# Performance work log

Hardware: AMD Instinct MI355X
Metric: run time of the kernel (lower is better)

## Reference

```python
import jax, jax.numpy as jnp
import numpy as np

B_SZ, SEQ, D_IN = 8, 4096, 1024
STATE, HEADS = 1024, 16
HEAD_DIM = STATE // HEADS
LN_EPS = 1e-5


def setup_inputs() -> dict:
    key = jax.random.key(0)
    ks = jax.random.split(key, 10)
    inp = {
        "x": jax.random.normal(ks[0], (B_SZ, SEQ, D_IN), dtype=jnp.float32),
        "W_in": jax.random.normal(ks[1], (STATE, D_IN), dtype=jnp.float32) * (1.0 / np.sqrt(D_IN)),
        "b_in": jnp.zeros((STATE,), dtype=jnp.float32),
        "log_A": jax.random.normal(ks[2], (HEADS, HEAD_DIM), dtype=jnp.float32) * 0.1 + 0.1,
        "B_p": jax.random.normal(ks[3], (HEADS, HEAD_DIM), dtype=jnp.float32) * 0.1 + 0.1,
        "C_p": jax.random.normal(ks[4], (HEADS, HEAD_DIM), dtype=jnp.float32) * 0.1 + 0.1,
        "W_out": jax.random.normal(ks[5], (STATE, STATE), dtype=jnp.float32) * (1.0 / np.sqrt(STATE)),
        "b_out": jnp.zeros((STATE,), dtype=jnp.float32),
        "gamma": jnp.ones((STATE,), dtype=jnp.float32),
        "beta": jnp.zeros((STATE,), dtype=jnp.float32),
    }
    return inp


def reference(x, W_in, b_in, log_A, B_p, C_p, W_out, b_out, gamma, beta):
    Bsz, S, _ = x.shape
    H, Dh = log_A.shape
    # input projection: (B,S,state)
    h = jnp.einsum("bsd,ed->bse", x, W_in) + b_in
    h = h.reshape(Bsz, S, H, Dh)
    decay = jnp.exp(-jax.nn.softplus(log_A))  # (H,Dh), time-invariant

    def step(s, xt):  # s,xt: (B,H,Dh)
        s = s * decay + B_p * xt
        return s, C_p * s

    s0 = jnp.zeros((Bsz, H, Dh), dtype=h.dtype)
    _, ys = jax.lax.scan(step, s0, jnp.swapaxes(h, 0, 1))  # ys: (S,B,H,Dh)
    y = jnp.swapaxes(ys, 0, 1).reshape(Bsz, S, H * Dh)
    out = jnp.einsum("bse,fe->bsf", y, W_out) + b_out
    # dropout in eval mode = identity; layer norm over last dim
    mu = out.mean(-1, keepdims=True)
    var = out.var(-1, keepdims=True)
    return (out - mu) * jax.lax.rsqrt(var + LN_EPS) * gamma + beta
```

## Files before the change

### kernel.cpp

```cpp
#include <hip/hip_runtime.h>

#define B_SZ  8
#define SEQ   4096
#define D_IN  1024
#define STATE 1024
#define M_TOT (B_SZ * SEQ)
#define LN_EPS 1e-5f
#define GK    1024
#define GN    1024

#define SCAN_L 128
#define SCAN_W 64

typedef short short8_t __attribute__((ext_vector_type(8)));
typedef float f32x4 __attribute__((ext_vector_type(4)));

__device__ __forceinline__ unsigned short f2bf(float f) {
  union { float f; unsigned u; } v; v.f = f;
  unsigned r = v.u + 0x7fffu + ((v.u >> 16) & 1u);
  return (unsigned short)(r >> 16);
}
__device__ __forceinline__ float bf2f(unsigned short h) {
  union { unsigned u; float f; } v; v.u = ((unsigned)h) << 16;
  return v.f;
}

__device__ __forceinline__ void gload16(const void* g, void* l) {
  __builtin_amdgcn_global_load_lds(
      (const __attribute__((address_space(1))) void*)g,
      (__attribute__((address_space(3))) void*)l, 16, 0, 0);
}

#define BAR()    __builtin_amdgcn_s_barrier()
#define SCHED0() __builtin_amdgcn_sched_barrier(0)

__device__ __forceinline__ void glue_pre_mfma() { SCHED0(); BAR(); SCHED0(); }
__device__ __forceinline__ void close_phase()   { SCHED0(); BAR(); SCHED0(); }

__global__ __launch_bounds__(256) void cast_kernel(const float* __restrict__ in,
                                                   unsigned short* __restrict__ out,
                                                   int n4) {
  int i = blockIdx.x * 256 + threadIdx.x;
  if (i < n4) {
    float4 v = ((const float4*)in)[i];
    ushort4 o;
    o.x = f2bf(v.x); o.y = f2bf(v.y); o.z = f2bf(v.z); o.w = f2bf(v.w);
    ((ushort4*)out)[i] = o;
  }
}


__device__ __forceinline__ void stage(const char* gbase, char* dbase, int t, int q) {
  gload16(gbase + (q * 131072 + t * 128), dbase + q * 8192);
}

template <int H, int NH, bool RDA, bool RDB>
__device__ __forceinline__ void phase_reads(const char* pAk0, const char* pAk1,
                                            const char* pBk0, const char* pBk1,
                                            short8_t (&a)[4][2], short8_t (&b)[2][2]) {
  if (RDB) {
#pragma unroll
    for (int nf = 0; nf < 2; nf++)
      b[nf][0] = *(const short8_t*)(pBk0 + ((NH * 32 + nf * 16) << 7));
  }
  if (RDA) {
#pragma unroll
    for (int mf = 0; mf < 4; mf++)
      a[mf][0] = *(const short8_t*)(pAk0 + ((H * 64 + mf * 16) << 7));
  }
  if (RDB) {
#pragma unroll
    for (int nf = 0; nf < 2; nf++)
      b[nf][1] = *(const short8_t*)(pBk1 + ((NH * 32 + nf * 16) << 7));
  }
  if (RDA) {
#pragma unroll
    for (int mf = 0; mf < 4; mf++)
      a[mf][1] = *(const short8_t*)(pAk1 + ((H * 64 + mf * 16) << 7));
  }
}

template <int H, int NH>
__device__ __forceinline__ void phase_mfma(short8_t (&a)[4][2], short8_t (&b)[2][2],
                                           f32x4 (&acc)[8][4]) {
  __builtin_amdgcn_s_setprio(1);
#pragma unroll
  for (int ks = 0; ks < 2; ks++)
#pragma unroll
    for (int mf = 0; mf < 4; mf++)
#pragma unroll
      for (int nf = 0; nf < 2; nf++)
        acc[H * 4 + mf][NH * 2 + nf] = __builtin_amdgcn_mfma_f32_16x16x32_bf16(
            a[mf][ks], b[nf][ks], acc[H * 4 + mf][NH * 2 + nf], 0, 0, 0);
  __builtin_amdgcn_s_setprio(0);
}

__global__ __launch_bounds__(512, 2) void gemm256(
    const unsigned short* __restrict__ A,
    const unsigned short* __restrict__ Bt,
    const float* __restrict__ bias,
    unsigned short* __restrict__ C,
    int M) {
  __shared__ __attribute__((aligned(16))) unsigned short As[2][256 * 64];
  __shared__ __attribute__((aligned(16))) unsigned short Bs[2][256 * 64];

  const int tid = threadIdx.x;
  const int w = tid >> 6, lane = tid & 63;
  const int wm = w >> 2, wn = w & 3;
  const int fr = lane & 15;
  const int fkb = (lane >> 4) * 16;

  const int nwg = gridDim.x;
  const int cpx = nwg >> 3;
  const int bid = blockIdx.x;
  const int wg = (bid & 7) * cpx + (bid >> 3);
  const int nbx = GN >> 8;
  const long m0 = (long)(wg / nbx) * 256;
  const long n0 = (long)(wg % nbx) * 256;

  const int xorv = (fr & 7) << 4;
  const int lo0 = (fr * 128 + 0  + fkb) ^ xorv;
  const int lo1 = (fr * 128 + 64 + fkb) ^ xorv;
  const char* pA0k0 = (const char*)&As[0][0] + wm * 16384 + lo0;
  const char* pA0k1 = (const char*)&As[0][0] + wm * 16384 + lo1;
  const char* pA1k0 = (const char*)&As[1][0] + wm * 16384 + lo0;
  const char* pA1k1 = (const char*)&As[1][0] + wm * 16384 + lo1;
  const char* pB0k0 = (const char*)&Bs[0][0] + wn * 8192 + lo0;
  const char* pB0k1 = (const char*)&Bs[0][0] + wn * 8192 + lo1;
  const char* pB1k0 = (const char*)&Bs[1][0] + wn * 8192 + lo0;
  const char* pB1k1 = (const char*)&Bs[1][0] + wn * 8192 + lo1;

  const int srow = tid >> 3;
  const int c2 = ((tid & 7) * 16) ^ ((srow & 7) << 4);
  const char* gA0 = (const char*)(A  + (m0 + srow) * (long)GK) + c2;
  const char* gB0 = (const char*)(Bt + (n0 + srow) * (long)GK) + c2;
  char* dA0 = (char*)&As[0][0] + ((tid >> 6) << 10);
  char* dA1 = (char*)&As[1][0] + ((tid >> 6) << 10);
  char* dB0 = (char*)&Bs[0][0] + ((tid >> 6) << 10);
  char* dB1 = (char*)&Bs[1][0] + ((tid >> 6) << 10);

  short8_t a[4][2], b[2][2];
  f32x4 acc[8][4] = {};

  const int nit = (GK >> 6) >> 1;

#pragma unroll
  for (int q = 0; q < 4; q++) stage(gA0, dA0, 0, q);
#pragma unroll
  for (int q = 0; q < 4; q++) stage(gB0, dB0, 0, q);
  SCHED0();
  asm volatile("s_waitcnt vmcnt(0)" ::: "memory");
  SCHED0(); BAR(); SCHED0();

#pragma unroll 1
  for (int i = 0; i < nit; ++i) {
    const bool last = (i == nit - 1);
    const int t1 = 2 * i + 1, t2 = 2 * i + 2;

    phase_reads<0, 0, true, true>(pA0k0, pA0k1, pB0k0, pB0k1, a, b);
#pragma unroll
    for (int q = 0; q < 4; q++) stage(gA0, dA1, t1, q);
    glue_pre_mfma();
    phase_mfma<0, 0>(a, b, acc);
    close_phase();

    phase_reads<0, 1, false, true>(pA0k0, pA0k1, pB0k0, pB0k1, a, b);
#pragma unroll
    for (int q = 0; q < 4; q++) stage(gB0, dB1, t1, q);
    glue_pre_mfma();
    phase_mfma<0, 1>(a, b, acc);
    close_phase();

    phase_reads<1, 1, true, false>(pA0k0, pA0k1, pB0k0, pB0k1, a, b);
    glue_pre_mfma();
    phase_mfma<1, 1>(a, b, acc);
    close_phase();

    phase_reads<1, 0, false, true>(pA0k0, pA0k1, pB0k0, pB0k1, a, b);
    glue_pre_mfma();
    phase_mfma<1, 0>(a, b, acc);
    SCHED0();
    asm volatile("s_waitcnt vmcnt(0)" ::: "memory");
    close_phase();

    phase_reads<0, 0, true, true>(pA1k0, pA1k1, pB1k0, pB1k1, a, b);
    if (!last) {
#pragma unroll
      for (int q = 0; q < 4; q++) stage(gA0, dA0, t2, q);
    }
    glue_pre_mfma();
    phase_mfma<0, 0>(a, b, acc);
    close_phase();

    phase_reads<0, 1, false, true>(pA1k0, pA1k1, pB1k0, pB1k1, a, b);
    if (!last) {
#pragma unroll
      for (int q = 0; q < 4; q++) stage(gB0, dB0, t2, q);
    }
    glue_pre_mfma();
    phase_mfma<0, 1>(a, b, acc);
    close_phase();

    phase_reads<1, 1, true, false>(pA1k0, pA1k1, pB1k0, pB1k1, a, b);
    glue_pre_mfma();
    phase_mfma<1, 1>(a, b, acc);
    close_phase();

    phase_reads<1, 0, false, true>(pA1k0, pA1k1, pB1k0, pB1k1, a, b);
    glue_pre_mfma();
    phase_mfma<1, 0>(a, b, acc);
    if (!last) {
      SCHED0();
      asm volatile("s_waitcnt vmcnt(0)" ::: "memory");
    }
    close_phase();
  }

  const int cc = lane & 15;
  const int cr = (lane >> 4) * 4;
  char* epi = (w < 4) ? ((char*)&As[0][0] + w * 16384)
                      : ((char*)&Bs[0][0] + (w - 4) * 16384);
  float bv[4];
#pragma unroll
  for (int nf = 0; nf < 4; nf++) bv[nf] = bias[n0 + wn * 64 + nf * 16 + cc];
#pragma unroll
  for (int mf = 0; mf < 8; mf++) {
#pragma unroll
    for (int r = 0; r < 4; r++) {
      const int row = mf * 16 + cr + r;
      const int rx = (row & 7) << 4;
#pragma unroll
      for (int nf = 0; nf < 4; nf++) {
        const int off = (row * 128 + (nf * 16 + cc) * 2) ^ rx;
        *(unsigned short*)(epi + off) = f2bf(acc[mf][nf][r] + bv[nf]);
      }
    }
  }
  const int rr = lane >> 3;
  const int rdoff = (lane * 16) ^ ((rr & 7) << 4);
  char* cbase = (char*)C + (m0 + wm * 128) * (GN * 2) + n0 * 2 + wn * 128 + (lane & 7) * 16;
#pragma unroll
  for (int s = 0; s < 16; s++) {
    short8_t vv = *(const short8_t*)(epi + s * 1024 + rdoff);
    *(short8_t*)(cbase + (long)(s * 8 + rr) * (GN * 2)) = vv;
  }
}

__global__ __launch_bounds__(256) void scan_kernel(
    const unsigned short* __restrict__ h,
    const float* __restrict__ log_A,
    const float* __restrict__ Bp,
    const float* __restrict__ Cp,
    unsigned short* __restrict__ y) {
  const int e = blockIdx.x * 256 + threadIdx.x;
  const int chunk = blockIdx.y;
  const int b = blockIdx.z;
  const float la = log_A[e];
  const float d = expf(-log1pf(expf(la)));
  const float bp = Bp[e];
  const float cp = Cp[e];
  const long base = ((long)b * SEQ) * STATE + e;
  const int t0 = chunk * SCAN_L;
  const int tw = (t0 >= SCAN_W) ? (t0 - SCAN_W) : 0;
  float s = 0.f;
  for (int t = tw; t < t0; ++t)
    s = fmaf(s, d, bp * bf2f(h[base + (long)t * STATE]));
  for (int t = t0; t < t0 + SCAN_L; ++t) {
    s = fmaf(s, d, bp * bf2f(h[base + (long)t * STATE]));
    y[base + (long)t * STATE] = f2bf(cp * s);
  }
}

__global__ __launch_bounds__(256) void ln_kernel(
    const unsigned short* __restrict__ X,
    const float* __restrict__ gamma,
    const float* __restrict__ beta,
    float* __restrict__ out) {
  const int row = blockIdx.x;
  const int tid = threadIdx.x;
  const long base = (long)row * STATE;
  ushort4 v = *(const ushort4*)&X[base + tid * 4];
  float x0 = bf2f(v.x), x1 = bf2f(v.y), x2 = bf2f(v.z), x3 = bf2f(v.w);
  float s = x0 + x1 + x2 + x3;
  float q = x0 * x0 + x1 * x1 + x2 * x2 + x3 * x3;
#pragma unroll
  for (int o = 32; o > 0; o >>= 1) {
    s += __shfl_xor(s, o);
    q += __shfl_xor(q, o);
  }
  __shared__ float sw[4], qw[4];
  const int wave = tid >> 6, lane = tid & 63;
  if (lane == 0) { sw[wave] = s; qw[wave] = q; }
  __syncthreads();
  s = sw[0] + sw[1] + sw[2] + sw[3];
  q = qw[0] + qw[1] + qw[2] + qw[3];
  const float mu = s * (1.0f / STATE);
  const float var = q * (1.0f / STATE) - mu * mu;
  const float inv = rsqrtf(var + LN_EPS);
  const int c = tid * 4;
  float4 o;
  o.x = (x0 - mu) * inv * gamma[c + 0] + beta[c + 0];
  o.y = (x1 - mu) * inv * gamma[c + 1] + beta[c + 1];
  o.z = (x2 - mu) * inv * gamma[c + 2] + beta[c + 2];
  o.w = (x3 - mu) * inv * gamma[c + 3] + beta[c + 3];
  *(float4*)&out[base + tid * 4] = o;
}

extern "C" void kernel_launch(void* const* d_in, const int* in_sizes, int n_in,
                              void* d_out, int out_size, void* d_ws, size_t ws_size,
                              hipStream_t stream) {
  const float* x     = (const float*)d_in[0];
  const float* W_in  = (const float*)d_in[1];
  const float* b_in  = (const float*)d_in[2];
  const float* log_A = (const float*)d_in[3];
  const float* Bp    = (const float*)d_in[4];
  const float* Cp    = (const float*)d_in[5];
  const float* W_out = (const float*)d_in[6];
  const float* b_out = (const float*)d_in[7];
  const float* gamma = (const float*)d_in[8];
  const float* beta  = (const float*)d_in[9];
  float* out = (float*)d_out;

  char* ws = (char*)d_ws;
  unsigned short* Wi_b = (unsigned short*)(ws);
  unsigned short* Wo_b = (unsigned short*)(ws + (2ull << 20));
  unsigned short* xb   = (unsigned short*)(ws + (4ull << 20));
  unsigned short* hb   = (unsigned short*)(ws + (68ull << 20));

  cast_kernel<<<(M_TOT * D_IN / 4) / 256, 256, 0, stream>>>(x, xb, M_TOT * D_IN / 4);
  cast_kernel<<<(STATE * D_IN / 4) / 256, 256, 0, stream>>>(W_in, Wi_b, STATE * D_IN / 4);
  cast_kernel<<<(STATE * STATE / 4) / 256, 256, 0, stream>>>(W_out, Wo_b, STATE * STATE / 4);

  gemm256<<<dim3((GN / 256) * (M_TOT / 256)), 512, 0, stream>>>(
      xb, Wi_b, b_in, hb, M_TOT);

  scan_kernel<<<dim3(STATE / 256, SEQ / SCAN_L, B_SZ), 256, 0, stream>>>(
      hb, log_A, Bp, Cp, xb);

  gemm256<<<dim3((GN / 256) * (M_TOT / 256)), 512, 0, stream>>>(
      xb, Wo_b, b_out, hb, M_TOT);

  ln_kernel<<<M_TOT, 256, 0, stream>>>(hb, gamma, beta, out);
}
```

Baseline: 265.6 us.

## Software-pipeline LDS fragment reads with MFMA using register double buffering

Restructures the GEMM main loop so the LDS fragment reads for the next MFMA phase are issued before the current phase's MFMAs. Separate register sets (aE/aO, b0/b1/b2) hold the fragments, and each phase now has one barrier instead of two. The A tile for the next odd step is prefetched one phase earlier, with a partial vmcnt wait. This is meant to hide LDS read latency and cut barrier overhead. In exchange it raises register pressure, which could hurt occupancy at 2 waves per SIMD, and the buffer reuse ordering is more fragile.

Measured after the change: 266.9 us. Within noise of the previous version (+0.5%).

```diff
diff --git a/kernel.cpp b/kernel.cpp
--- a/kernel.cpp
+++ b/kernel.cpp
@@ -33,9 +33,6 @@
 
 #define BAR()    __builtin_amdgcn_s_barrier()
 #define SCHED0() __builtin_amdgcn_sched_barrier(0)
-
-__device__ __forceinline__ void glue_pre_mfma() { SCHED0(); BAR(); SCHED0(); }
-__device__ __forceinline__ void close_phase()   { SCHED0(); BAR(); SCHED0(); }
 
 __global__ __launch_bounds__(256) void cast_kernel(const float* __restrict__ in,
                                                    unsigned short* __restrict__ out,
@@ -54,35 +51,28 @@
   gload16(gbase + (q * 131072 + t * 128), dbase + q * 8192);
 }
 
-template <int H, int NH, bool RDA, bool RDB>
-__device__ __forceinline__ void phase_reads(const char* pAk0, const char* pAk1,
-                                            const char* pBk0, const char* pBk1,
-                                            short8_t (&a)[4][2], short8_t (&b)[2][2]) {
-  if (RDB) {
-#pragma unroll
-    for (int nf = 0; nf < 2; nf++)
-      b[nf][0] = *(const short8_t*)(pBk0 + ((NH * 32 + nf * 16) << 7));
-  }
-  if (RDA) {
-#pragma unroll
-    for (int mf = 0; mf < 4; mf++)
-      a[mf][0] = *(const short8_t*)(pAk0 + ((H * 64 + mf * 16) << 7));
-  }
-  if (RDB) {
-#pragma unroll
-    for (int nf = 0; nf < 2; nf++)
-      b[nf][1] = *(const short8_t*)(pBk1 + ((NH * 32 + nf * 16) << 7));
-  }
-  if (RDA) {
-#pragma unroll
-    for (int mf = 0; mf < 4; mf++)
-      a[mf][1] = *(const short8_t*)(pAk1 + ((H * 64 + mf * 16) << 7));
+template <int H>
+__device__ __forceinline__ void readA(const char* pk0, const char* pk1,
+                                      short8_t (&a)[4][2]) {
+#pragma unroll
+  for (int mf = 0; mf < 4; mf++) {
+    a[mf][0] = *(const short8_t*)(pk0 + ((H * 64 + mf * 16) << 7));
+    a[mf][1] = *(const short8_t*)(pk1 + ((H * 64 + mf * 16) << 7));
+  }
+}
+template <int NH>
+__device__ __forceinline__ void readB(const char* pk0, const char* pk1,
+                                      short8_t (&b)[2][2]) {
+#pragma unroll
+  for (int nf = 0; nf < 2; nf++) {
+    b[nf][0] = *(const short8_t*)(pk0 + ((NH * 32 + nf * 16) << 7));
+    b[nf][1] = *(const short8_t*)(pk1 + ((NH * 32 + nf * 16) << 7));
   }
 }
 
 template <int H, int NH>
-__device__ __forceinline__ void phase_mfma(short8_t (&a)[4][2], short8_t (&b)[2][2],
-                                           f32x4 (&acc)[8][4]) {
+__device__ __forceinline__ void mfma16(short8_t (&a)[4][2], short8_t (&b)[2][2],
+                                       f32x4 (&acc)[8][4]) {
   __builtin_amdgcn_s_setprio(1);
 #pragma unroll
   for (int ks = 0; ks < 2; ks++)
@@ -139,7 +129,7 @@
   char* dB0 = (char*)&Bs[0][0] + ((tid >> 6) << 10);
   char* dB1 = (char*)&Bs[1][0] + ((tid >> 6) << 10);
 
-  short8_t a[4][2], b[2][2];
+  short8_t aE[4][2], aO[4][2], b0[2][2], b1[2][2], b2[2][2];
   f32x4 acc[8][4] = {};
 
   const int nit = (GK >> 6) >> 1;
@@ -148,72 +138,78 @@
   for (int q = 0; q < 4; q++) stage(gA0, dA0, 0, q);
 #pragma unroll
   for (int q = 0; q < 4; q++) stage(gB0, dB0, 0, q);
+#pragma unroll
+  for (int q = 0; q < 4; q++) stage(gA0, dA1, 1, q);
   SCHED0();
-  asm volatile("s_waitcnt vmcnt(0)" ::: "memory");
-  SCHED0(); BAR(); SCHED0();
+  asm volatile("s_waitcnt vmcnt(4)" ::: "memory");
+  BAR();
+  readA<0>(pA0k0, pA0k1, aE);
+  readB<0>(pB0k0, pB0k1, b0);
 
 #pragma unroll 1
   for (int i = 0; i < nit; ++i) {
     const bool last = (i == nit - 1);
-    const int t1 = 2 * i + 1, t2 = 2 * i + 2;
-
-    phase_reads<0, 0, true, true>(pA0k0, pA0k1, pB0k0, pB0k1, a, b);
-#pragma unroll
-    for (int q = 0; q < 4; q++) stage(gA0, dA1, t1, q);
-    glue_pre_mfma();
-    phase_mfma<0, 0>(a, b, acc);
-    close_phase();
-
-    phase_reads<0, 1, false, true>(pA0k0, pA0k1, pB0k0, pB0k1, a, b);
+    const int t1 = 2 * i + 1, t2 = 2 * i + 2, t3 = 2 * i + 3;
+
+    readB<1>(pB0k0, pB0k1, b1);
 #pragma unroll
     for (int q = 0; q < 4; q++) stage(gB0, dB1, t1, q);
-    glue_pre_mfma();
-    phase_mfma<0, 1>(a, b, acc);
-    close_phase();
-
-    phase_reads<1, 1, true, false>(pA0k0, pA0k1, pB0k0, pB0k1, a, b);
-    glue_pre_mfma();
-    phase_mfma<1, 1>(a, b, acc);
-    close_phase();
-
-    phase_reads<1, 0, false, true>(pA0k0, pA0k1, pB0k0, pB0k1, a, b);
-    glue_pre_mfma();
-    phase_mfma<1, 0>(a, b, acc);
-    SCHED0();
+    SCHED0();
+    mfma16<0, 0>(aE, b0, acc);
+    BAR();
+
+    readA<1>(pA0k0, pA0k1, aO);
+    SCHED0();
+    mfma16<0, 1>(aE, b1, acc);
+    BAR();
+
+    readB<0>(pB0k0, pB0k1, b2);
+    SCHED0();
+    mfma16<1, 1>(aO, b1, acc);
     asm volatile("s_waitcnt vmcnt(0)" ::: "memory");
-    close_phase();
-
-    phase_reads<0, 0, true, true>(pA1k0, pA1k1, pB1k0, pB1k1, a, b);
+    BAR();
+
+    readA<0>(pA1k0, pA1k1, aE);
+    readB<0>(pB1k0, pB1k1, b0);
     if (!last) {
 #pragma unroll
       for (int q = 0; q < 4; q++) stage(gA0, dA0, t2, q);
     }
-    glue_pre_mfma();
-    phase_mfma<0, 0>(a, b, acc);
-    close_phase();
-
-    phase_reads<0, 1, false, true>(pA1k0, pA1k1, pB1k0, pB1k1, a, b);
+    SCHED0();
+    mfma16<1, 0>(aO, b2, acc);
+    BAR();
+
+    readB<1>(pB1k0, pB1k1, b1);
     if (!last) {
 #pragma unroll
       for (int q = 0; q < 4; q++) stage(gB0, dB0, t2, q);
     }
-    glue_pre_mfma();
-    phase_mfma<0, 1>(a, b, acc);
-    close_phase();
-
-    phase_reads<1, 1, true, false>(pA1k0, pA1k1, pB1k0, pB1k1, a, b);
-    glue_pre_mfma();
-    phase_mfma<1, 1>(a, b, acc);
-    close_phase();
-
-    phase_reads<1, 0, false, true>(pA1k0, pA1k1, pB1k0, pB1k1, a, b);
-    glue_pre_mfma();
-    phase_mfma<1, 0>(a, b, acc);
+    SCHED0();
+    mfma16<0, 0>(aE, b0, acc);
+    BAR();
+
+    readA<1>(pA1k0, pA1k1, aO);
+    SCHED0();
+    mfma16<0, 1>(aE, b1, acc);
+    BAR();
+
+    readB<0>(pB1k0, pB1k1, b2);
+    SCHED0();
+    mfma16<1, 1>(aO, b1, acc);
     if (!last) {
-      SCHED0();
       asm volatile("s_waitcnt vmcnt(0)" ::: "memory");
     }
-    close_phase();
+    BAR();
+
+    if (!last) {
+      readA<0>(pA0k0, pA0k1, aE);
+      readB<0>(pB0k0, pB0k1, b0);
+#pragma unroll
+      for (int q = 0; q < 4; q++) stage(gA0, dA1, t3, q);
+    }
+    SCHED0();
+    mfma16<1, 0>(aO, b2, acc);
+    BAR();
   }
 
   const int cc = lane & 15;
```
